# Performance work log

Hardware: AMD Instinct MI355X
Metric: run time of the kernel (lower is better)

The kernel has to match this reference:

```python
import jax, jax.numpy as jnp
import numpy as np

B, T, D = 4, 2048, 1024
H, DH = 16, 64

def setup_inputs() -> dict:
    key = jax.random.key(0)
    k1, k2, k3 = jax.random.split(key, 3)
    x = jax.random.normal(k1, (B, T, D), dtype=jnp.float32)
    # nn.Linear weights stored [out, in]; we keep that convention
    w_attn = jax.random.normal(k2, (3 * D, D), dtype=jnp.float32) * (1.0 / np.sqrt(D))
    w_proj = jax.random.normal(k3, (D, D), dtype=jnp.float32) * (1.0 / np.sqrt(D))
    return {"x": x, "w_attn": w_attn, "w_proj": w_proj}

def reference(x, w_attn, w_proj):
    Bx, Tx, Dx = x.shape
    qkv = jnp.einsum('btd,ed->bte', x, w_attn)            # [B,T,3D]
    qkv = qkv.reshape(Bx, Tx, 3, H, DH)
    q = qkv[:, :, 0].transpose(0, 2, 1, 3)                # [B,H,T,DH]
    k = qkv[:, :, 1].transpose(0, 2, 1, 3)
    v = qkv[:, :, 2].transpose(0, 2, 1, 3)
    scale = 1.0 / np.sqrt(DH).astype(np.float32)
    att = jnp.einsum('bhqd,bhkd->bhqk', q, k) * scale     # [B,H,T,T]
    causal = jnp.tril(jnp.ones((Tx, Tx), dtype=bool))
    att = jnp.where(causal[None, None], att, jnp.float32(-jnp.inf))
    att = jax.nn.softmax(att, axis=-1)
    y = jnp.einsum('bhqk,bhkd->bhqd', att, v)             # [B,H,T,DH]
    y = y.transpose(0, 2, 1, 3).reshape(Bx, Tx, Dx)       # [B,T,D]
    y = jnp.einsum('btd,ed->bte', y, w_proj)
    return y
```

## Files before the change

kernel.cpp:

```cpp
#include <hip/hip_runtime.h>

typedef unsigned short u16;
typedef __bf16 bf16x8 __attribute__((ext_vector_type(8)));
typedef float floatx4 __attribute__((ext_vector_type(4)));

__device__ inline u16 f2bf(float x) {
    unsigned int u = __builtin_bit_cast(unsigned int, x);
    return (u16)((u + 0x7FFFu + ((u >> 16) & 1u)) >> 16);
}

__device__ inline floatx4 fzero() {
    floatx4 z = {0.f, 0.f, 0.f, 0.f};
    return z;
}

#if defined(__has_builtin)
#if __has_builtin(__builtin_amdgcn_exp2f)
#define EXP2F(x) __builtin_amdgcn_exp2f(x)
#endif
#endif
#ifndef EXP2F
#define EXP2F(x) exp2f(x)
#endif

template <bool F32>
__device__ inline bf16x8 ld8(const void* base, size_t off) {
    if constexpr (F32) {
        const float* p = (const float*)base + off;
        float4 a = *(const float4*)p;
        float4 b = *(const float4*)(p + 4);
        union { u16 u[8]; bf16x8 v; } t;
        t.u[0] = f2bf(a.x); t.u[1] = f2bf(a.y); t.u[2] = f2bf(a.z); t.u[3] = f2bf(a.w);
        t.u[4] = f2bf(b.x); t.u[5] = f2bf(b.y); t.u[6] = f2bf(b.z); t.u[7] = f2bf(b.w);
        return t.v;
    } else {
        return *(const bf16x8*)((const u16*)base + off);
    }
}

typedef __attribute__((address_space(1))) const unsigned int as1_u32;
typedef __attribute__((address_space(3))) unsigned int as3_u32;
__device__ inline void gld_lds16(const void* g, void* l) {
    __builtin_amdgcn_global_load_lds((as1_u32*)g, (as3_u32*)l, 16, 0, 0);
}

__device__ inline u16* swz_ptr(u16* buf, int row, int col) {
    return (u16*)((char*)buf + row * 128 + ((col * 2) ^ ((row & 7) << 4)));
}

__global__ __launch_bounds__(256) void cvt_f32_bf16(const float* __restrict__ src,
                                                    u16* __restrict__ dst, int n8) {
    int i = blockIdx.x * 256 + threadIdx.x;
    if (i >= n8) return;
    dst += (size_t)i * 8;
    *(bf16x8*)dst = ld8<true>(src, (size_t)i * 8);
}

#define BK 32

template <bool AF32, bool BF32, bool CF32>
__global__ __launch_bounds__(256) void gemm_bt(const void* __restrict__ Ap,
                                               const void* __restrict__ Bp,
                                               void* __restrict__ Cp,
                                               int M, int N, int K) {
    __shared__ alignas(16) u16 As[128 * BK];
    __shared__ alignas(16) u16 Bs[128 * BK];

    const int tid  = threadIdx.x;
    const int lane = tid & 63;
    const int wave = tid >> 6;
    const int wm = (wave >> 1) * 64;
    const int wn = (wave & 1) * 64;
    const int tm = blockIdx.y * 128;
    const int tn = blockIdx.x * 128;
    const int l15 = lane & 15;
    const int l4  = lane >> 4;

    const int srow = tid >> 2;
    const int scol = (tid & 3) * 8;

    floatx4 acc[4][4];
#pragma unroll
    for (int i = 0; i < 4; i++)
#pragma unroll
        for (int j = 0; j < 4; j++) acc[i][j] = fzero();

    const u16* Ag = nullptr;
    const u16* Bg = nullptr;
    if constexpr (!AF32 && !BF32) {
        Ag = (const u16*)Ap + (size_t)(tm + srow) * K + scol;
        Bg = (const u16*)Bp + (size_t)(tn + srow) * K + scol;
    }

    for (int k0 = 0; k0 < K; k0 += BK) {
        if constexpr (!AF32 && !BF32) {
            __syncthreads();
            gld_lds16(Ag + k0,                 &As[wave * 512]);
            gld_lds16(Ag + k0 + (size_t)64 * K, &As[2048 + wave * 512]);
            gld_lds16(Bg + k0,                 &Bs[wave * 512]);
            gld_lds16(Bg + k0 + (size_t)64 * K, &Bs[2048 + wave * 512]);
            __syncthreads();
        } else {
            bf16x8 av[2], bv[2];
#pragma unroll
            for (int q = 0; q < 2; q++) {
                av[q] = ld8<AF32>(Ap, (size_t)(tm + srow + q * 64) * K + k0 + scol);
                bv[q] = ld8<BF32>(Bp, (size_t)(tn + srow + q * 64) * K + k0 + scol);
            }
            __syncthreads();
#pragma unroll
            for (int q = 0; q < 2; q++) {
                *(bf16x8*)&As[(srow + q * 64) * BK + scol] = av[q];
                *(bf16x8*)&Bs[(srow + q * 64) * BK + scol] = bv[q];
            }
            __syncthreads();
        }

        bf16x8 af[4], bf[4];
#pragma unroll
        for (int i = 0; i < 4; i++)
            af[i] = *(const bf16x8*)&As[(wm + i * 16 + l15) * BK + l4 * 8];
#pragma unroll
        for (int j = 0; j < 4; j++)
            bf[j] = *(const bf16x8*)&Bs[(wn + j * 16 + l15) * BK + l4 * 8];
#pragma unroll
        for (int i = 0; i < 4; i++)
#pragma unroll
            for (int j = 0; j < 4; j++)
                acc[i][j] = __builtin_amdgcn_mfma_f32_16x16x32_bf16(af[i], bf[j], acc[i][j], 0, 0, 0);
    }

#pragma unroll
    for (int i = 0; i < 4; i++)
#pragma unroll
        for (int j = 0; j < 4; j++)
#pragma unroll
            for (int r = 0; r < 4; r++) {
                int row = tm + wm + i * 16 + l4 * 4 + r;
                int col = tn + wn + j * 16 + l15;
                if constexpr (CF32)
                    ((float*)Cp)[(size_t)row * N + col] = acc[i][j][r];
                else
                    ((u16*)Cp)[(size_t)row * N + col] = f2bf(acc[i][j][r]);
            }
}

__global__ __launch_bounds__(256) void transpose_v(const u16* __restrict__ qkv,
                                                   u16* __restrict__ vT) {
    __shared__ alignas(16) u16 Ts[64 * 80];
    const int bh = blockIdx.x;
    const int b = bh >> 4, h = bh & 15;
    const int t0 = blockIdx.y * 64;
    const int tid = threadIdx.x;
    const int r = tid >> 3;
    const int c = tid & 7;
#pragma unroll
    for (int p = 0; p < 2; p++) {
        int tr = r + p * 32;
        *(bf16x8*)&Ts[tr * 80 + c * 8] =
            *(const bf16x8*)&qkv[(size_t)(b * 2048 + t0 + tr) * 3072 + 2048 + h * 64 + c * 8];
    }
    __syncthreads();
#pragma unroll
    for (int p = 0; p < 2; p++) {
        int dr = r + p * 32;
        union { u16 u[8]; bf16x8 v; } t;
#pragma unroll
        for (int i = 0; i < 8; i++) t.u[i] = Ts[(c * 8 + i) * 80 + dr];
        *(bf16x8*)&vT[(size_t)bh * 131072 + (size_t)dr * 2048 + t0 + c * 8] = t.v;
    }
}

template <bool USE_VT>
__global__ __launch_bounds__(256) void attn2(const u16* __restrict__ qkv,
                                             const u16* __restrict__ vT,
                                             u16* __restrict__ y) {
    const int T = 2048, CW = 3072;
    __shared__ alignas(16) u16 KP[64 * 64];
    __shared__ alignas(16) u16 Vt[64 * 64];
    __shared__ alignas(16) u16 PB[64 * 64];

    const int tid  = threadIdx.x;
    const int lane = tid & 63;
    const int wave = tid >> 6;
    const int l15 = lane & 15;
    const int l4  = lane >> 4;

    const int bh = blockIdx.x;
    const int qt = 31 - blockIdx.y;
    const int b = bh >> 4, h = bh & 15;
    const int q0 = qt * 64;

    const size_t base = (size_t)b * T * CW + h * 64;
    const u16* qp = qkv + base;
    const u16* kp = qkv + base + 1024;
    const u16* vp = qkv + base + 2048;
    const u16* vtp = USE_VT ? (vT + (size_t)bh * 131072) : nullptr;

    bf16x8 qf[2];
    {
        int qrow = q0 + wave * 16 + l15;
        qf[0] = *(const bf16x8*)&qp[(size_t)qrow * CW + l4 * 8];
        qf[1] = *(const bf16x8*)&qp[(size_t)qrow * CW + 32 + l4 * 8];
    }

    const float C2 = 0.18033688f;
    float lrow[4] = {0.f, 0.f, 0.f, 0.f};
    floatx4 Oacc[4];
#pragma unroll
    for (int cf = 0; cf < 4; cf++) Oacc[cf] = fzero();

    const int sr = tid >> 3;
    const int sc = tid & 7;

    bf16x8 kreg[2], vreg[2];
    auto stage_load = [&](int kt) {
        const int t0 = kt * 64;
#pragma unroll
        for (int p = 0; p < 2; p++)
            kreg[p] = *(const bf16x8*)&kp[(size_t)(t0 + sr + p * 32) * CW + sc * 8];
        if constexpr (USE_VT) {
#pragma unroll
            for (int p = 0; p < 2; p++)
                vreg[p] = *(const bf16x8*)&vtp[(size_t)(sr + p * 32) * 2048 + t0 + sc * 8];
        } else {
            const int dh = tid & 63;
            const int tb = wave * 8;
#pragma unroll
            for (int p = 0; p < 2; p++) {
                union { u16 u[8]; bf16x8 v; } tmp;
#pragma unroll
                for (int i = 0; i < 8; i++)
                    tmp.u[i] = vp[(size_t)(t0 + tb + p * 32 + i) * CW + dh];
                vreg[p] = tmp.v;
            }
        }
    };

    stage_load(0);

    for (int kt = 0; kt <= qt; kt++) {
        const int t0 = kt * 64;
        __syncthreads();

#pragma unroll
        for (int p = 0; p < 2; p++)
            *(bf16x8*)swz_ptr(KP, sr + p * 32, sc * 8) = kreg[p];
        if constexpr (USE_VT) {
#pragma unroll
            for (int p = 0; p < 2; p++)
                *(bf16x8*)swz_ptr(Vt, sr + p * 32, sc * 8) = vreg[p];
        } else {
            const int dh = tid & 63;
            const int tb = wave * 8;
#pragma unroll
            for (int p = 0; p < 2; p++)
                *(bf16x8*)swz_ptr(Vt, dh, tb + p * 32) = vreg[p];
        }
        __syncthreads();

        if (kt < qt) stage_load(kt + 1);

#pragma unroll
        for (int j = 0; j < 4; j++) {
            bf16x8 k0f = *(const bf16x8*)swz_ptr(KP, j * 16 + l15, l4 * 8);
            bf16x8 k1f = *(const bf16x8*)swz_ptr(KP, j * 16 + l15, 32 + l4 * 8);
            floatx4 s = fzero();
            s = __builtin_amdgcn_mfma_f32_16x16x32_bf16(qf[0], k0f, s, 0, 0, 0);
            s = __builtin_amdgcn_mfma_f32_16x16x32_bf16(qf[1], k1f, s, 0, 0, 0);
            float pj[4];
            if (kt == qt) {
#pragma unroll
                for (int r = 0; r < 4; r++) {
                    int qrow = q0 + wave * 16 + l4 * 4 + r;
                    int krow = t0 + j * 16 + l15;
                    float e = (krow <= qrow) ? s[r] * C2 : -1.0e30f;
                    pj[r] = EXP2F(e);
                }
            } else {
#pragma unroll
                for (int r = 0; r < 4; r++) pj[r] = EXP2F(s[r] * C2);
            }
#pragma unroll
            for (int r = 0; r < 4; r++) lrow[r] += pj[r];
#pragma unroll
            for (int r = 0; r < 4; r++)
                *swz_ptr(PB, wave * 16 + l4 * 4 + r, j * 16 + l15) = f2bf(pj[r]);
        }

        bf16x8 pf0 = *(const bf16x8*)swz_ptr(PB, wave * 16 + l15, l4 * 8);
        bf16x8 pf1 = *(const bf16x8*)swz_ptr(PB, wave * 16 + l15, 32 + l4 * 8);
#pragma unroll
        for (int cf = 0; cf < 4; cf++) {
            bf16x8 v0f = *(const bf16x8*)swz_ptr(Vt, cf * 16 + l15, l4 * 8);
            bf16x8 v1f = *(const bf16x8*)swz_ptr(Vt, cf * 16 + l15, 32 + l4 * 8);
            Oacc[cf] = __builtin_amdgcn_mfma_f32_16x16x32_bf16(pf0, v0f, Oacc[cf], 0, 0, 0);
            Oacc[cf] = __builtin_amdgcn_mfma_f32_16x16x32_bf16(pf1, v1f, Oacc[cf], 0, 0, 0);
        }
    }

#pragma unroll
    for (int r = 0; r < 4; r++) {
#pragma unroll
        for (int off = 1; off < 16; off <<= 1)
            lrow[r] += __shfl_xor(lrow[r], off, 64);
    }
#pragma unroll
    for (int r = 0; r < 4; r++) {
        float inv = 1.0f / lrow[r];
        int qrow = q0 + wave * 16 + l4 * 4 + r;
        size_t orow = ((size_t)b * T + qrow) * 1024 + h * 64;
#pragma unroll
        for (int cf = 0; cf < 4; cf++)
            y[orow + cf * 16 + l15] = f2bf(Oacc[cf][r] * inv);
    }
}

extern "C" void kernel_launch(void* const* d_in, const int* in_sizes, int n_in,
                              void* d_out, int out_size, void* d_ws, size_t ws_size,
                              hipStream_t stream) {
    const float* x      = (const float*)d_in[0];
    const float* w_attn = (const float*)d_in[1];
    const float* w_proj = (const float*)d_in[2];
    float* out = (float*)d_out;

    const size_t QKV = (size_t)8192 * 3072;
    const size_t Y   = (size_t)8192 * 1024;
    const size_t VTE = (size_t)64 * 64 * 2048;
    const size_t XB  = (size_t)8192 * 1024;
    const size_t WAB = (size_t)3072 * 1024;
    const size_t WPB = (size_t)1024 * 1024;

    u16* qkv = (u16*)d_ws;
    u16* yb  = qkv + QKV;

    const bool full = ws_size >= (QKV + Y + VTE + XB + WAB + WPB) * sizeof(u16);
    const bool mid  = ws_size >= (QKV + Y + VTE) * sizeof(u16);
    if (ws_size < (QKV + Y) * sizeof(u16)) return;

    dim3 blk(256);
    dim3 g1(3072 / 128, 8192 / 128), g2(1024 / 128, 8192 / 128);
    dim3 ga(64, 32);

    if (full) {
        u16* vT  = yb + Y;
        u16* xb  = vT + VTE;
        u16* wab = xb + XB;
        u16* wpb = wab + WAB;
        cvt_f32_bf16<<<(XB / 8 + 255) / 256, blk, 0, stream>>>(x, xb, (int)(XB / 8));
        cvt_f32_bf16<<<(WAB / 8 + 255) / 256, blk, 0, stream>>>(w_attn, wab, (int)(WAB / 8));
        cvt_f32_bf16<<<(WPB / 8 + 255) / 256, blk, 0, stream>>>(w_proj, wpb, (int)(WPB / 8));
        gemm_bt<false, false, false><<<g1, blk, 0, stream>>>(xb, wab, qkv, 8192, 3072, 1024);
        transpose_v<<<ga, blk, 0, stream>>>(qkv, vT);
        attn2<true><<<ga, blk, 0, stream>>>(qkv, vT, yb);
        gemm_bt<false, false, true><<<g2, blk, 0, stream>>>(yb, wpb, out, 8192, 1024, 1024);
    } else if (mid) {
        u16* vT = yb + Y;
        gemm_bt<true, true, false><<<g1, blk, 0, stream>>>(x, w_attn, qkv, 8192, 3072, 1024);
        transpose_v<<<ga, blk, 0, stream>>>(qkv, vT);
        attn2<true><<<ga, blk, 0, stream>>>(qkv, vT, yb);
        gemm_bt<false, true, true><<<g2, blk, 0, stream>>>(yb, w_proj, out, 8192, 1024, 1024);
    } else {
        gemm_bt<true, true, false><<<g1, blk, 0, stream>>>(x, w_attn, qkv, 8192, 3072, 1024);
        attn2<false><<<ga, blk, 0, stream>>>(qkv, nullptr, yb);
        gemm_bt<false, true, true><<<g2, blk, 0, stream>>>(yb, w_proj, out, 8192, 1024, 1024);
    }
}
```

Before: 270.5 us.

## Double-buffer GEMM and attention LDS loads, process 128 query rows per block

The bf16 GEMM path gets double-buffered LDS tiles, so the async global-to-LDS load of the next K slice overlaps the MFMA work on the current one and each iteration needs one barrier instead of two. The attention kernel becomes attn3: each block covers 128 query rows (two 64-row groups), and K and V^T tiles are double-buffered through direct global-to-LDS loads with a pre-swizzled source column. Every staged K/V tile is then reused by two query groups, and masking is only applied on diagonal tiles. In exchange, LDS use roughly doubles, which may lower occupancy, and the attention grid halves to 1024 blocks with uneven causal work per block.

```diff
diff --git a/kernel.cpp b/kernel.cpp
--- a/kernel.cpp
+++ b/kernel.cpp
@@ -63,8 +63,8 @@
                                                const void* __restrict__ Bp,
                                                void* __restrict__ Cp,
                                                int M, int N, int K) {
-    __shared__ alignas(16) u16 As[128 * BK];
-    __shared__ alignas(16) u16 Bs[128 * BK];
+    __shared__ alignas(16) u16 As[2][128 * BK];
+    __shared__ alignas(16) u16 Bs[2][128 * BK];
 
     const int tid  = threadIdx.x;
     const int lane = tid & 63;
@@ -85,22 +85,42 @@
 #pragma unroll
         for (int j = 0; j < 4; j++) acc[i][j] = fzero();
 
-    const u16* Ag = nullptr;
-    const u16* Bg = nullptr;
     if constexpr (!AF32 && !BF32) {
-        Ag = (const u16*)Ap + (size_t)(tm + srow) * K + scol;
-        Bg = (const u16*)Bp + (size_t)(tn + srow) * K + scol;
-    }
-
-    for (int k0 = 0; k0 < K; k0 += BK) {
-        if constexpr (!AF32 && !BF32) {
+        const u16* Ag = (const u16*)Ap + (size_t)(tm + srow) * K + scol;
+        const u16* Bg = (const u16*)Bp + (size_t)(tn + srow) * K + scol;
+
+        auto stage = [&](int buf, int k0) {
+            gld_lds16(Ag + k0,                  &As[buf][wave * 512]);
+            gld_lds16(Ag + k0 + (size_t)64 * K, &As[buf][2048 + wave * 512]);
+            gld_lds16(Bg + k0,                  &Bs[buf][wave * 512]);
+            gld_lds16(Bg + k0 + (size_t)64 * K, &Bs[buf][2048 + wave * 512]);
+        };
+
+        stage(0, 0);
+        __syncthreads();
+        int cur = 0;
+        const int nk = K / BK;
+        for (int t = 0; t < nk; t++) {
+            if (t + 1 < nk) stage(cur ^ 1, (t + 1) * BK);
+
+            bf16x8 af[4], bfv[4];
+#pragma unroll
+            for (int i = 0; i < 4; i++)
+                af[i] = *(const bf16x8*)&As[cur][(wm + i * 16 + l15) * BK + l4 * 8];
+#pragma unroll
+            for (int j = 0; j < 4; j++)
+                bfv[j] = *(const bf16x8*)&Bs[cur][(wn + j * 16 + l15) * BK + l4 * 8];
+#pragma unroll
+            for (int i = 0; i < 4; i++)
+#pragma unroll
+                for (int j = 0; j < 4; j++)
+                    acc[i][j] = __builtin_amdgcn_mfma_f32_16x16x32_bf16(af[i], bfv[j], acc[i][j], 0, 0, 0);
+
             __syncthreads();
-            gld_lds16(Ag + k0,                 &As[wave * 512]);
-            gld_lds16(Ag + k0 + (size_t)64 * K, &As[2048 + wave * 512]);
-            gld_lds16(Bg + k0,                 &Bs[wave * 512]);
-            gld_lds16(Bg + k0 + (size_t)64 * K, &Bs[2048 + wave * 512]);
-            __syncthreads();
-        } else {
+            cur ^= 1;
+        }
+    } else {
+        for (int k0 = 0; k0 < K; k0 += BK) {
             bf16x8 av[2], bv[2];
 #pragma unroll
             for (int q = 0; q < 2; q++) {
@@ -110,24 +130,24 @@
             __syncthreads();
 #pragma unroll
             for (int q = 0; q < 2; q++) {
-                *(bf16x8*)&As[(srow + q * 64) * BK + scol] = av[q];
-                *(bf16x8*)&Bs[(srow + q * 64) * BK + scol] = bv[q];
+                *(bf16x8*)&As[0][(srow + q * 64) * BK + scol] = av[q];
+                *(bf16x8*)&Bs[0][(srow + q * 64) * BK + scol] = bv[q];
             }
             __syncthreads();
-        }
-
-        bf16x8 af[4], bf[4];
-#pragma unroll
-        for (int i = 0; i < 4; i++)
-            af[i] = *(const bf16x8*)&As[(wm + i * 16 + l15) * BK + l4 * 8];
-#pragma unroll
-        for (int j = 0; j < 4; j++)
-            bf[j] = *(const bf16x8*)&Bs[(wn + j * 16 + l15) * BK + l4 * 8];
-#pragma unroll
-        for (int i = 0; i < 4; i++)
+
+            bf16x8 af[4], bfv[4];
+#pragma unroll
+            for (int i = 0; i < 4; i++)
+                af[i] = *(const bf16x8*)&As[0][(wm + i * 16 + l15) * BK + l4 * 8];
 #pragma unroll
             for (int j = 0; j < 4; j++)
-                acc[i][j] = __builtin_amdgcn_mfma_f32_16x16x32_bf16(af[i], bf[j], acc[i][j], 0, 0, 0);
+                bfv[j] = *(const bf16x8*)&Bs[0][(wn + j * 16 + l15) * BK + l4 * 8];
+#pragma unroll
+            for (int i = 0; i < 4; i++)
+#pragma unroll
+                for (int j = 0; j < 4; j++)
+                    acc[i][j] = __builtin_amdgcn_mfma_f32_16x16x32_bf16(af[i], bfv[j], acc[i][j], 0, 0, 0);
+        }
     }
 
 #pragma unroll
@@ -171,14 +191,13 @@
     }
 }
 
-template <bool USE_VT>
-__global__ __launch_bounds__(256) void attn2(const u16* __restrict__ qkv,
+__global__ __launch_bounds__(256) void attn3(const u16* __restrict__ qkv,
                                              const u16* __restrict__ vT,
                                              u16* __restrict__ y) {
     const int T = 2048, CW = 3072;
-    __shared__ alignas(16) u16 KP[64 * 64];
-    __shared__ alignas(16) u16 Vt[64 * 64];
-    __shared__ alignas(16) u16 PB[64 * 64];
+    __shared__ alignas(16) u16 Kb[2][64 * 64];
+    __shared__ alignas(16) u16 Vb[2][64 * 64];
+    __shared__ alignas(16) u16 PB[128 * 64];
 
     const int tid  = threadIdx.x;
     const int lane = tid & 63;
@@ -187,6 +206,159 @@
     const int l4  = lane >> 4;
 
     const int bh = blockIdx.x;
+    const int qt = 15 - blockIdx.y;
+    const int b = bh >> 4, h = bh & 15;
+    const int q0 = qt * 128;
+    const int nkt = 2 * qt + 2;
+
+    const size_t base = (size_t)b * T * CW + h * 64;
+    const u16* qp = qkv + base;
+    const u16* kp = qkv + base + 1024;
+    const u16* vtp = vT + (size_t)bh * 131072;
+
+    bf16x8 qf[2][2];
+#pragma unroll
+    for (int g = 0; g < 2; g++) {
+        int qrow = q0 + g * 64 + wave * 16 + l15;
+        qf[g][0] = *(const bf16x8*)&qp[(size_t)qrow * CW + l4 * 8];
+        qf[g][1] = *(const bf16x8*)&qp[(size_t)qrow * CW + 32 + l4 * 8];
+    }
+
+    const float C2 = 0.18033688f;
+    float lrow[2][4];
+    floatx4 Oacc[2][4];
+#pragma unroll
+    for (int g = 0; g < 2; g++)
+#pragma unroll
+        for (int cf = 0; cf < 4; cf++) { Oacc[g][cf] = fzero(); lrow[g][cf] = 0.f; }
+
+    const int sr = tid >> 3;
+    const int sc = tid & 7;
+    const int ssc = sc ^ (sr & 7);
+
+    auto stage = [&](int buf, int kt) {
+        const int t0 = kt * 64;
+#pragma unroll
+        for (int p = 0; p < 2; p++)
+            gld_lds16(&kp[(size_t)(t0 + sr + p * 32) * CW + ssc * 8],
+                      &Kb[buf][p * 2048 + wave * 512]);
+#pragma unroll
+        for (int p = 0; p < 2; p++)
+            gld_lds16(&vtp[(size_t)(sr + p * 32) * 2048 + t0 + ssc * 8],
+                      &Vb[buf][p * 2048 + wave * 512]);
+    };
+
+    stage(0, 0);
+    __syncthreads();
+    int cur = 0;
+
+    const int rbase0 = q0 + wave * 16;
+    const int rbase1 = q0 + 64 + wave * 16;
+
+    for (int kt = 0; kt < nkt; kt++) {
+        const int t0 = kt * 64;
+        if (kt + 1 < nkt) stage(cur ^ 1, kt + 1);
+
+        u16* KP = Kb[cur];
+        u16* Vt = Vb[cur];
+
+        const bool act0 = (t0 <= rbase0 + 15);
+        const bool act1 = (t0 <= rbase1 + 15);
+        const bool dia0 = (t0 + 63 > rbase0);
+        const bool dia1 = (t0 + 63 > rbase1);
+
+#pragma unroll
+        for (int j = 0; j < 4; j++) {
+            bf16x8 k0f = *(const bf16x8*)swz_ptr(KP, j * 16 + l15, l4 * 8);
+            bf16x8 k1f = *(const bf16x8*)swz_ptr(KP, j * 16 + l15, 32 + l4 * 8);
+#pragma unroll
+            for (int g = 0; g < 2; g++) {
+                const bool act = g ? act1 : act0;
+                if (!act) continue;
+                const bool dia = g ? dia1 : dia0;
+                const int rbase = g ? rbase1 : rbase0;
+                floatx4 s = fzero();
+                s = __builtin_amdgcn_mfma_f32_16x16x32_bf16(qf[g][0], k0f, s, 0, 0, 0);
+                s = __builtin_amdgcn_mfma_f32_16x16x32_bf16(qf[g][1], k1f, s, 0, 0, 0);
+                float pj[4];
+                if (dia) {
+#pragma unroll
+                    for (int r = 0; r < 4; r++) {
+                        int qrow = rbase + l4 * 4 + r;
+                        int krow = t0 + j * 16 + l15;
+                        float e = (krow <= qrow) ? s[r] * C2 : -1.0e30f;
+                        pj[r] = EXP2F(e);
+                    }
+                } else {
+#pragma unroll
+                    for (int r = 0; r < 4; r++) pj[r] = EXP2F(s[r] * C2);
+                }
+#pragma unroll
+                for (int r = 0; r < 4; r++) lrow[g][r] += pj[r];
+#pragma unroll
+                for (int r = 0; r < 4; r++)
+                    *swz_ptr(PB, g * 64 + wave * 16 + l4 * 4 + r, j * 16 + l15) = f2bf(pj[r]);
+            }
+        }
+
+        bf16x8 pf[2][2];
+#pragma unroll
+        for (int g = 0; g < 2; g++) {
+            if (!(g ? act1 : act0)) continue;
+            pf[g][0] = *(const bf16x8*)swz_ptr(PB, g * 64 + wave * 16 + l15, l4 * 8);
+            pf[g][1] = *(const bf16x8*)swz_ptr(PB, g * 64 + wave * 16 + l15, 32 + l4 * 8);
+        }
+#pragma unroll
+        for (int cf = 0; cf < 4; cf++) {
+            bf16x8 v0f = *(const bf16x8*)swz_ptr(Vt, cf * 16 + l15, l4 * 8);
+            bf16x8 v1f = *(const bf16x8*)swz_ptr(Vt, cf * 16 + l15, 32 + l4 * 8);
+#pragma unroll
+            for (int g = 0; g < 2; g++) {
+                if (!(g ? act1 : act0)) continue;
+                Oacc[g][cf] = __builtin_amdgcn_mfma_f32_16x16x32_bf16(pf[g][0], v0f, Oacc[g][cf], 0, 0, 0);
+                Oacc[g][cf] = __builtin_amdgcn_mfma_f32_16x16x32_bf16(pf[g][1], v1f, Oacc[g][cf], 0, 0, 0);
+            }
+        }
+
+        __syncthreads();
+        cur ^= 1;
+    }
+
+#pragma unroll
+    for (int g = 0; g < 2; g++)
+#pragma unroll
+        for (int r = 0; r < 4; r++) {
+#pragma unroll
+            for (int off = 1; off < 16; off <<= 1)
+                lrow[g][r] += __shfl_xor(lrow[g][r], off, 64);
+        }
+#pragma unroll
+    for (int g = 0; g < 2; g++)
+#pragma unroll
+        for (int r = 0; r < 4; r++) {
+            float inv = 1.0f / lrow[g][r];
+            int qrow = q0 + g * 64 + wave * 16 + l4 * 4 + r;
+            size_t orow = ((size_t)b * T + qrow) * 1024 + h * 64;
+#pragma unroll
+            for (int cf = 0; cf < 4; cf++)
+                y[orow + cf * 16 + l15] = f2bf(Oacc[g][cf][r] * inv);
+        }
+}
+
+__global__ __launch_bounds__(256) void attn_gather(const u16* __restrict__ qkv,
+                                                   u16* __restrict__ y) {
+    const int T = 2048, CW = 3072;
+    __shared__ alignas(16) u16 KP[64 * 64];
+    __shared__ alignas(16) u16 Vt[64 * 64];
+    __shared__ alignas(16) u16 PB[64 * 64];
+
+    const int tid  = threadIdx.x;
+    const int lane = tid & 63;
+    const int wave = tid >> 6;
+    const int l15 = lane & 15;
+    const int l4  = lane >> 4;
+
+    const int bh = blockIdx.x;
     const int qt = 31 - blockIdx.y;
     const int b = bh >> 4, h = bh & 15;
     const int q0 = qt * 64;
@@ -195,7 +367,6 @@
     const u16* qp = qkv + base;
     const u16* kp = qkv + base + 1024;
     const u16* vp = qkv + base + 2048;
-    const u16* vtp = USE_VT ? (vT + (size_t)bh * 131072) : nullptr;
 
     bf16x8 qf[2];
     {
@@ -219,21 +390,15 @@
 #pragma unroll
         for (int p = 0; p < 2; p++)
             kreg[p] = *(const bf16x8*)&kp[(size_t)(t0 + sr + p * 32) * CW + sc * 8];
-        if constexpr (USE_VT) {
-#pragma unroll
-            for (int p = 0; p < 2; p++)
-                vreg[p] = *(const bf16x8*)&vtp[(size_t)(sr + p * 32) * 2048 + t0 + sc * 8];
-        } else {
-            const int dh = tid & 63;
-            const int tb = wave * 8;
-#pragma unroll
-            for (int p = 0; p < 2; p++) {
-                union { u16 u[8]; bf16x8 v; } tmp;
-#pragma unroll
-                for (int i = 0; i < 8; i++)
-                    tmp.u[i] = vp[(size_t)(t0 + tb + p * 32 + i) * CW + dh];
-                vreg[p] = tmp.v;
-            }
+        const int dh = tid & 63;
+        const int tb = wave * 8;
+#pragma unroll
+        for (int p = 0; p < 2; p++) {
+            union { u16 u[8]; bf16x8 v; } tmp;
+#pragma unroll
+            for (int i = 0; i < 8; i++)
+                tmp.u[i] = vp[(size_t)(t0 + tb + p * 32 + i) * CW + dh];
+            vreg[p] = tmp.v;
         }
     };
 
@@ -242,15 +407,10 @@
     for (int kt = 0; kt <= qt; kt++) {
         const int t0 = kt * 64;
         __syncthreads();
-
 #pragma unroll
         for (int p = 0; p < 2; p++)
             *(bf16x8*)swz_ptr(KP, sr + p * 32, sc * 8) = kreg[p];
-        if constexpr (USE_VT) {
-#pragma unroll
-            for (int p = 0; p < 2; p++)
-                *(bf16x8*)swz_ptr(Vt, sr + p * 32, sc * 8) = vreg[p];
-        } else {
+        {
             const int dh = tid & 63;
             const int tb = wave * 8;
 #pragma unroll
@@ -340,7 +500,8 @@
 
     dim3 blk(256);
     dim3 g1(3072 / 128, 8192 / 128), g2(1024 / 128, 8192 / 128);
-    dim3 ga(64, 32);
+    dim3 ga(64, 16);
+    dim3 gt(64, 32);
 
     if (full) {
         u16* vT  = yb + Y;
@@ -351,18 +512,18 @@
         cvt_f32_bf16<<<(WAB / 8 + 255) / 256, blk, 0, stream>>>(w_attn, wab, (int)(WAB / 8));
         cvt_f32_bf16<<<(WPB / 8 + 255) / 256, blk, 0, stream>>>(w_proj, wpb, (int)(WPB / 8));
         gemm_bt<false, false, false><<<g1, blk, 0, stream>>>(xb, wab, qkv, 8192, 3072, 1024);
-        transpose_v<<<ga, blk, 0, stream>>>(qkv, vT);
-        attn2<true><<<ga, blk, 0, stream>>>(qkv, vT, yb);
+        transpose_v<<<gt, blk, 0, stream>>>(qkv, vT);
+        attn3<<<ga, blk, 0, stream>>>(qkv, vT, yb);
         gemm_bt<false, false, true><<<g2, blk, 0, stream>>>(yb, wpb, out, 8192, 1024, 1024);
     } else if (mid) {
         u16* vT = yb + Y;
         gemm_bt<true, true, false><<<g1, blk, 0, stream>>>(x, w_attn, qkv, 8192, 3072, 1024);
-        transpose_v<<<ga, blk, 0, stream>>>(qkv, vT);
-        attn2<true><<<ga, blk, 0, stream>>>(qkv, vT, yb);
+        transpose_v<<<gt, blk, 0, stream>>>(qkv, vT);
+        attn3<<<ga, blk, 0, stream>>>(qkv, vT, yb);
         gemm_bt<false, true, true><<<g2, blk, 0, stream>>>(yb, w_proj, out, 8192, 1024, 1024);
     } else {
         gemm_bt<true, true, false><<<g1, blk, 0, stream>>>(x, w_attn, qkv, 8192, 3072, 1024);
-        attn2<false><<<ga, blk, 0, stream>>>(qkv, nullptr, yb);
+        attn_gather<<<gt, blk, 0, stream>>>(qkv, yb);
         gemm_bt<false, true, true><<<g2, blk, 0, stream>>>(yb, w_proj, out, 8192, 1024, 1024);
     }
 }
```

After: 282.3 us. 4.3% more time.

## Double-buffer LDS tiles in bf16 GEMM and merge conversion kernels into one launch

Applied to the files above, without the earlier changes.

The bf16 GEMM path now uses two LDS buffers, so the async global-to-LDS loads for the next K tile are issued before the MFMAs on the current tile, with one barrier per iteration instead of two. This is meant to overlap load latency with compute, at the cost of doubled LDS usage (32KB per block), which may reduce occupancy. The three f32-to-bf16 conversion launches are also fused into a single launch that picks the source by index, removing launch overhead.

```diff
diff --git a/kernel.cpp b/kernel.cpp
--- a/kernel.cpp
+++ b/kernel.cpp
@@ -48,12 +48,17 @@
     return (u16*)((char*)buf + row * 128 + ((col * 2) ^ ((row & 7) << 4)));
 }
 
-__global__ __launch_bounds__(256) void cvt_f32_bf16(const float* __restrict__ src,
-                                                    u16* __restrict__ dst, int n8) {
+__global__ __launch_bounds__(256) void cvt_all(const float* __restrict__ x,
+                                               const float* __restrict__ wa,
+                                               const float* __restrict__ wp,
+                                               u16* __restrict__ dst) {
+    const int XB8 = 1048576, WAB8 = 393216;
     int i = blockIdx.x * 256 + threadIdx.x;
-    if (i >= n8) return;
-    dst += (size_t)i * 8;
-    *(bf16x8*)dst = ld8<true>(src, (size_t)i * 8);
+    const float* src; size_t off;
+    if (i < XB8)             { src = x;  off = (size_t)i * 8; }
+    else if (i < XB8 + WAB8) { src = wa; off = (size_t)(i - XB8) * 8; }
+    else                     { src = wp; off = (size_t)(i - XB8 - WAB8) * 8; }
+    *(bf16x8*)(dst + (size_t)i * 8) = ld8<true>(src, off);
 }
 
 #define BK 32
@@ -63,8 +68,8 @@
                                                const void* __restrict__ Bp,
                                                void* __restrict__ Cp,
                                                int M, int N, int K) {
-    __shared__ alignas(16) u16 As[128 * BK];
-    __shared__ alignas(16) u16 Bs[128 * BK];
+    __shared__ alignas(16) u16 As[2][128 * BK];
+    __shared__ alignas(16) u16 Bs[2][128 * BK];
 
     const int tid  = threadIdx.x;
     const int lane = tid & 63;
@@ -85,22 +90,42 @@
 #pragma unroll
         for (int j = 0; j < 4; j++) acc[i][j] = fzero();
 
-    const u16* Ag = nullptr;
-    const u16* Bg = nullptr;
     if constexpr (!AF32 && !BF32) {
-        Ag = (const u16*)Ap + (size_t)(tm + srow) * K + scol;
-        Bg = (const u16*)Bp + (size_t)(tn + srow) * K + scol;
-    }
-
-    for (int k0 = 0; k0 < K; k0 += BK) {
-        if constexpr (!AF32 && !BF32) {
+        const u16* Ag = (const u16*)Ap + (size_t)(tm + srow) * K + scol;
+        const u16* Bg = (const u16*)Bp + (size_t)(tn + srow) * K + scol;
+
+        auto stage = [&](int buf, int k0) {
+            gld_lds16(Ag + k0,                  &As[buf][wave * 512]);
+            gld_lds16(Ag + k0 + (size_t)64 * K, &As[buf][2048 + wave * 512]);
+            gld_lds16(Bg + k0,                  &Bs[buf][wave * 512]);
+            gld_lds16(Bg + k0 + (size_t)64 * K, &Bs[buf][2048 + wave * 512]);
+        };
+
+        stage(0, 0);
+        __syncthreads();
+        int cur = 0;
+        const int nk = K / BK;
+        for (int t = 0; t < nk; t++) {
+            if (t + 1 < nk) stage(cur ^ 1, (t + 1) * BK);
+
+            bf16x8 af[4], bfv[4];
+#pragma unroll
+            for (int i = 0; i < 4; i++)
+                af[i] = *(const bf16x8*)&As[cur][(wm + i * 16 + l15) * BK + l4 * 8];
+#pragma unroll
+            for (int j = 0; j < 4; j++)
+                bfv[j] = *(const bf16x8*)&Bs[cur][(wn + j * 16 + l15) * BK + l4 * 8];
+#pragma unroll
+            for (int i = 0; i < 4; i++)
+#pragma unroll
+                for (int j = 0; j < 4; j++)
+                    acc[i][j] = __builtin_amdgcn_mfma_f32_16x16x32_bf16(af[i], bfv[j], acc[i][j], 0, 0, 0);
+
             __syncthreads();
-            gld_lds16(Ag + k0,                 &As[wave * 512]);
-            gld_lds16(Ag + k0 + (size_t)64 * K, &As[2048 + wave * 512]);
-            gld_lds16(Bg + k0,                 &Bs[wave * 512]);
-            gld_lds16(Bg + k0 + (size_t)64 * K, &Bs[2048 + wave * 512]);
-            __syncthreads();
-        } else {
+            cur ^= 1;
+        }
+    } else {
+        for (int k0 = 0; k0 < K; k0 += BK) {
             bf16x8 av[2], bv[2];
 #pragma unroll
             for (int q = 0; q < 2; q++) {
@@ -110,24 +135,24 @@
             __syncthreads();
 #pragma unroll
             for (int q = 0; q < 2; q++) {
-                *(bf16x8*)&As[(srow + q * 64) * BK + scol] = av[q];
-                *(bf16x8*)&Bs[(srow + q * 64) * BK + scol] = bv[q];
+                *(bf16x8*)&As[0][(srow + q * 64) * BK + scol] = av[q];
+                *(bf16x8*)&Bs[0][(srow + q * 64) * BK + scol] = bv[q];
             }
             __syncthreads();
-        }
-
-        bf16x8 af[4], bf[4];
-#pragma unroll
-        for (int i = 0; i < 4; i++)
-            af[i] = *(const bf16x8*)&As[(wm + i * 16 + l15) * BK + l4 * 8];
-#pragma unroll
-        for (int j = 0; j < 4; j++)
-            bf[j] = *(const bf16x8*)&Bs[(wn + j * 16 + l15) * BK + l4 * 8];
-#pragma unroll
-        for (int i = 0; i < 4; i++)
+
+            bf16x8 af[4], bfv[4];
+#pragma unroll
+            for (int i = 0; i < 4; i++)
+                af[i] = *(const bf16x8*)&As[0][(wm + i * 16 + l15) * BK + l4 * 8];
 #pragma unroll
             for (int j = 0; j < 4; j++)
-                acc[i][j] = __builtin_amdgcn_mfma_f32_16x16x32_bf16(af[i], bf[j], acc[i][j], 0, 0, 0);
+                bfv[j] = *(const bf16x8*)&Bs[0][(wn + j * 16 + l15) * BK + l4 * 8];
+#pragma unroll
+            for (int i = 0; i < 4; i++)
+#pragma unroll
+                for (int j = 0; j < 4; j++)
+                    acc[i][j] = __builtin_amdgcn_mfma_f32_16x16x32_bf16(af[i], bfv[j], acc[i][j], 0, 0, 0);
+        }
     }
 
 #pragma unroll
@@ -345,11 +370,9 @@
     if (full) {
         u16* vT  = yb + Y;
         u16* xb  = vT + VTE;
+        cvt_all<<<6144, blk, 0, stream>>>(x, w_attn, w_proj, xb);
         u16* wab = xb + XB;
         u16* wpb = wab + WAB;
-        cvt_f32_bf16<<<(XB / 8 + 255) / 256, blk, 0, stream>>>(x, xb, (int)(XB / 8));
-        cvt_f32_bf16<<<(WAB / 8 + 255) / 256, blk, 0, stream>>>(w_attn, wab, (int)(WAB / 8));
-        cvt_f32_bf16<<<(WPB / 8 + 255) / 256, blk, 0, stream>>>(w_proj, wpb, (int)(WPB / 8));
         gemm_bt<false, false, false><<<g1, blk, 0, stream>>>(xb, wab, qkv, 8192, 3072, 1024);
         transpose_v<<<ga, blk, 0, stream>>>(qkv, vT);
         attn2<true><<<ga, blk, 0, stream>>>(qkv, vT, yb);
```

Measured after the change: 255.9 us. 5.4% less time.
